# Optimization experiments

Measured on AMD Instinct MI355X. Metric: run time of the kernel, lower is better.

Reference implementation:

```python
import jax, jax.numpy as jnp
import numpy as np

B, S, E, H = 4, 2048, 512, 8
DH = E // H
EPS = 1e-5

def _ln(x, g, b):
    m = jnp.mean(x, axis=-1, keepdims=True)
    v = jnp.var(x, axis=-1, keepdims=True)
    return (x - m) * jax.lax.rsqrt(v + EPS) * g + b

def setup_inputs() -> dict:
    key = jax.random.key(0)
    ks = jax.random.split(key, 8)
    sc = 0.02
    return {
        "x": jax.random.normal(ks[0], (B, S, E), dtype=jnp.float32),
        "ln1_g": jnp.ones((E,), jnp.float32),
        "ln1_b": jnp.zeros((E,), jnp.float32),
        "in_proj_w": sc * jax.random.normal(ks[1], (3 * E, E), jnp.float32),
        "in_proj_b": jnp.zeros((3 * E,), jnp.float32),
        "out_w": sc * jax.random.normal(ks[2], (E, E), jnp.float32),
        "out_b": jnp.zeros((E,), jnp.float32),
        "ln2_g": jnp.ones((E,), jnp.float32),
        "ln2_b": jnp.zeros((E,), jnp.float32),
        "fc1_w": sc * jax.random.normal(ks[3], (E, E), jnp.float32),
        "fc1_b": jnp.zeros((E,), jnp.float32),
        "fc2_w": sc * jax.random.normal(ks[4], (E, E), jnp.float32),
        "fc2_b": jnp.zeros((E,), jnp.float32),
    }

def reference(x, ln1_g, ln1_b, in_proj_w, in_proj_b, out_w, out_b,
              ln2_g, ln2_b, fc1_w, fc1_b, fc2_w, fc2_b):
    # pre-LN
    z = _ln(x, ln1_g, ln1_b)
    # qkv projection (torch MHA packed in_proj: [3E, E])
    qkv = z @ in_proj_w.T + in_proj_b          # [B,S,3E]
    q, k, v = jnp.split(qkv, 3, axis=-1)
    q = q.reshape(B, S, H, DH)
    k = k.reshape(B, S, H, DH)
    v = v.reshape(B, S, H, DH)
    scores = jnp.einsum("bqhd,bkhd->bhqk", q, k) / np.sqrt(DH).astype(np.float32)
    causal = jnp.triu(jnp.ones((S, S), dtype=bool), k=1)  # True = masked
    neg = jnp.finfo(scores.dtype).min
    scores = jnp.where(causal, neg, scores)
    attn = jax.nn.softmax(scores, axis=-1)      # [B,H,S,S]
    ctx = jnp.einsum("bhqk,bkhd->bqhd", attn, v).reshape(B, S, E)
    attn_out = ctx @ out_w.T + out_b
    # torch MHA with need_weights=True averages over heads by default
    attn_weights = jnp.mean(attn, axis=1)       # [B,S,S]
    z2 = x + attn_out
    y = _ln(z2, ln2_g, ln2_b)
    y = jax.nn.leaky_relu(y @ fc1_w.T + fc1_b, negative_slope=0.01)
    y = y @ fc2_w.T + fc2_b
    y = y + z2
    return (y, attn_weights)
```

## Files before the change

kernel.cpp:

```cpp
#include <hip/hip_runtime.h>

typedef short bf16x8 __attribute__((ext_vector_type(8)));
typedef float f32x4 __attribute__((ext_vector_type(4)));
typedef unsigned short u16x8 __attribute__((ext_vector_type(8)));

#define NB 4
#define SQ 2048
#define EM 512
#define NH 8
#define DHD 64
#define QSCALE 0.1803368801111731f

__device__ __forceinline__ unsigned short f2bf(float x) {
  unsigned u = __float_as_uint(x);
  u += 0x7FFFu + ((u >> 16) & 1u);
  return (unsigned short)(u >> 16);
}

__device__ __forceinline__ int sw8(int row, int col8) { return col8 ^ ((row & 7) << 3); }

__global__ __launch_bounds__(256) void f2bf_kernel(const float* __restrict__ in,
                                                   unsigned short* __restrict__ out, int n) {
  int i = (blockIdx.x * 256 + threadIdx.x) * 8;
  if (i >= n) return;
  f32x4 a = *(const f32x4*)(in + i);
  f32x4 b = *(const f32x4*)(in + i + 4);
  u16x8 o;
#pragma unroll
  for (int j = 0; j < 4; ++j) { o[j] = f2bf(a[j]); o[j + 4] = f2bf(b[j]); }
  *(u16x8*)(out + i) = o;
}

__global__ __launch_bounds__(256) void ln_kernel(const float* __restrict__ x,
                                                 const float* __restrict__ g,
                                                 const float* __restrict__ bb,
                                                 unsigned short* __restrict__ out) {
  int tid = threadIdx.x;
  int row = blockIdx.x * 4 + (tid >> 6);
  int lane = tid & 63;
  size_t base = (size_t)row * EM + lane * 8;
  f32x4 v0 = *(const f32x4*)(x + base);
  f32x4 v1 = *(const f32x4*)(x + base + 4);
  float s = 0.f, q = 0.f;
#pragma unroll
  for (int j = 0; j < 4; ++j) { s += v0[j] + v1[j]; q += v0[j] * v0[j] + v1[j] * v1[j]; }
#pragma unroll
  for (int m = 1; m < 64; m <<= 1) { s += __shfl_xor(s, m); q += __shfl_xor(q, m); }
  float mean = s * (1.f / EM);
  float var = q * (1.f / EM) - mean * mean;
  float rs = rsqrtf(var + 1e-5f);
  f32x4 g0 = *(const f32x4*)(g + lane * 8), g1 = *(const f32x4*)(g + lane * 8 + 4);
  f32x4 b0 = *(const f32x4*)(bb + lane * 8), b1 = *(const f32x4*)(bb + lane * 8 + 4);
  u16x8 o;
#pragma unroll
  for (int j = 0; j < 4; ++j) {
    o[j] = f2bf((v0[j] - mean) * rs * g0[j] + b0[j]);
    o[j + 4] = f2bf((v1[j] - mean) * rs * g1[j] + b1[j]);
  }
  *(u16x8*)(out + base) = o;
}

template <bool LEAKY, bool RESID, bool OUTF32, bool QKV>
__global__ __launch_bounds__(256) void gemm64(
    const unsigned short* __restrict__ A, const unsigned short* __restrict__ Bm,
    const float* __restrict__ bias, const float* __restrict__ resid,
    float* __restrict__ outf, unsigned short* __restrict__ outh,
    unsigned short* __restrict__ qo, unsigned short* __restrict__ ko,
    unsigned short* __restrict__ vo, int M, int N, int K) {
  __shared__ unsigned short As[64][64];
  __shared__ unsigned short Bs[64][64];
  int m0 = blockIdx.x * 64, n0 = blockIdx.y * 64;
  int t = threadIdx.x;
  int ar = t >> 2, ac = (t & 3) * 16;
  int wv = t >> 6, ln = t & 63, lg = ln >> 4, lr = ln & 15;
  f32x4 acc[4];
#pragma unroll
  for (int c = 0; c < 4; ++c)
#pragma unroll
    for (int r = 0; r < 4; ++r) acc[c][r] = 0.f;

  const unsigned short* ag = A + (size_t)(m0 + ar) * K + ac;
  const unsigned short* bg = Bm + (size_t)(n0 + ar) * K + ac;
  for (int k0 = 0; k0 < K; k0 += 64) {
    u16x8 a0 = *(const u16x8*)(ag + k0);
    u16x8 a1 = *(const u16x8*)(ag + k0 + 8);
    u16x8 b0 = *(const u16x8*)(bg + k0);
    u16x8 b1 = *(const u16x8*)(bg + k0 + 8);
    *(u16x8*)&As[ar][sw8(ar, ac)] = a0;
    *(u16x8*)&As[ar][sw8(ar, ac + 8)] = a1;
    *(u16x8*)&Bs[ar][sw8(ar, ac)] = b0;
    *(u16x8*)&Bs[ar][sw8(ar, ac + 8)] = b1;
    __syncthreads();
#pragma unroll
    for (int kk = 0; kk < 64; kk += 32) {
      int arw = wv * 16 + lr;
      bf16x8 af = *(const bf16x8*)&As[arw][sw8(arw, kk + lg * 8)];
#pragma unroll
      for (int c = 0; c < 4; ++c) {
        int brw = c * 16 + lr;
        bf16x8 bf = *(const bf16x8*)&Bs[brw][sw8(brw, kk + lg * 8)];
        acc[c] = __builtin_amdgcn_mfma_f32_16x16x32_bf16(af, bf, acc[c], 0, 0, 0);
      }
    }
    __syncthreads();
  }
#pragma unroll
  for (int c = 0; c < 4; ++c) {
    int C_ = n0 + c * 16 + lr;
    float bv = bias[C_];
#pragma unroll
    for (int r = 0; r < 4; ++r) {
      int R_ = m0 + wv * 16 + lg * 4 + r;
      float v = acc[c][r] + bv;
      if (LEAKY) v = v > 0.f ? v : 0.01f * v;
      if (RESID) v += resid[(size_t)R_ * N + C_];
      if (QKV) {
        int which = C_ >> 9, f = C_ & 511, h = f >> 6, d = f & 63;
        int b_ = R_ >> 11, s_ = R_ & 2047;
        if (which == 0) {
          qo[(((size_t)b_ * NH + h) * SQ + s_) * DHD + d] = f2bf(v * QSCALE);
        } else if (which == 1) {
          ko[(((size_t)b_ * NH + h) * SQ + s_) * DHD + d] = f2bf(v);
        } else {
          vo[(((size_t)b_ * NH + h) * DHD + d) * SQ + s_] = f2bf(v);
        }
      } else if (OUTF32) {
        outf[(size_t)R_ * N + C_] = v;
      } else {
        outh[(size_t)R_ * N + C_] = f2bf(v);
      }
    }
  }
}

__global__ __launch_bounds__(256) void flash_kernel(
    const unsigned short* __restrict__ Q, const unsigned short* __restrict__ Kb,
    const unsigned short* __restrict__ Vt, unsigned short* __restrict__ ctx,
    float* __restrict__ mstat, float* __restrict__ lstat) {
  __shared__ unsigned short Ks[2][64][64];
  __shared__ unsigned short Vs[2][64][64];
  __shared__ unsigned short Ps[4][16][64];
  int h = blockIdx.y, b = blockIdx.z;
  int t = threadIdx.x, wv = t >> 6, ln = t & 63, lg = ln >> 4, lr = ln & 15;
  int ar = t >> 2, ac = (t & 3) * 16;
  size_t headoff = ((size_t)b * NH + h) * SQ;
  const unsigned short* kgb = Kb + (headoff + ar) * DHD + ac;
  const unsigned short* vgb = Vt + (((size_t)b * NH + h) * DHD + ar) * SQ + ac;

  bf16x8 vones;
#pragma unroll
  for (int j = 0; j < 8; ++j) vones[j] = (lr == 0) ? (short)0x3F80 : (short)0;

  for (int half = 0; half < 2; ++half) {
    int qt = half ? blockIdx.x : (31 - blockIdx.x);
    int qb = qt * 64;
    const unsigned short* qrow = Q + (headoff + qb + wv * 16 + lr) * DHD;
    bf16x8 aq0 = *(const bf16x8*)(qrow + lg * 8);
    bf16x8 aq1 = *(const bf16x8*)(qrow + 32 + lg * 8);

    f32x4 cacc[4], lacc;
#pragma unroll
    for (int nd = 0; nd < 4; ++nd)
#pragma unroll
      for (int r = 0; r < 4; ++r) cacc[nd][r] = 0.f;
#pragma unroll
    for (int r = 0; r < 4; ++r) lacc[r] = 0.f;
    float mrun[4];
#pragma unroll
    for (int r = 0; r < 4; ++r) mrun[r] = -__builtin_inff();

    int nkt = qt + 1;
    __syncthreads();
    u16x8 kr0 = *(const u16x8*)(kgb);
    u16x8 kr1 = *(const u16x8*)(kgb + 8);
    u16x8 vr0 = *(const u16x8*)(vgb);
    u16x8 vr1 = *(const u16x8*)(vgb + 8);
    *(u16x8*)&Ks[0][ar][sw8(ar, ac)] = kr0;
    *(u16x8*)&Ks[0][ar][sw8(ar, ac + 8)] = kr1;
    *(u16x8*)&Vs[0][ar][sw8(ar, ac)] = vr0;
    *(u16x8*)&Vs[0][ar][sw8(ar, ac + 8)] = vr1;
    if (nkt > 1) {
      kr0 = *(const u16x8*)(kgb + (size_t)64 * DHD);
      kr1 = *(const u16x8*)(kgb + (size_t)64 * DHD + 8);
      vr0 = *(const u16x8*)(vgb + 64);
      vr1 = *(const u16x8*)(vgb + 64 + 8);
    }

    for (int kt = 0; kt < nkt; ++kt) {
      int cur = kt & 1;
      __syncthreads();
      if (kt + 1 < nkt) {
        int nb = cur ^ 1;
        *(u16x8*)&Ks[nb][ar][sw8(ar, ac)] = kr0;
        *(u16x8*)&Ks[nb][ar][sw8(ar, ac + 8)] = kr1;
        *(u16x8*)&Vs[nb][ar][sw8(ar, ac)] = vr0;
        *(u16x8*)&Vs[nb][ar][sw8(ar, ac + 8)] = vr1;
        if (kt + 2 < nkt) {
          size_t ko2 = (size_t)(kt + 2) * 64;
          kr0 = *(const u16x8*)(kgb + ko2 * DHD);
          kr1 = *(const u16x8*)(kgb + ko2 * DHD + 8);
          vr0 = *(const u16x8*)(vgb + ko2);
          vr1 = *(const u16x8*)(vgb + ko2 + 8);
        }
      }

      float sv[4][4];
      __builtin_amdgcn_s_setprio(1);
#pragma unroll
      for (int nt = 0; nt < 4; ++nt) {
        f32x4 sf;
#pragma unroll
        for (int r = 0; r < 4; ++r) sf[r] = 0.f;
        int brw = nt * 16 + lr;
        bf16x8 bk0 = *(const bf16x8*)&Ks[cur][brw][sw8(brw, lg * 8)];
        bf16x8 bk1 = *(const bf16x8*)&Ks[cur][brw][sw8(brw, 32 + lg * 8)];
        sf = __builtin_amdgcn_mfma_f32_16x16x32_bf16(aq0, bk0, sf, 0, 0, 0);
        sf = __builtin_amdgcn_mfma_f32_16x16x32_bf16(aq1, bk1, sf, 0, 0, 0);
#pragma unroll
        for (int r = 0; r < 4; ++r) sv[nt][r] = sf[r];
      }
      __builtin_amdgcn_s_setprio(0);
      if (kt == nkt - 1) {
        int kbase = kt * 64;
#pragma unroll
        for (int nt = 0; nt < 4; ++nt) {
          int kcol = kbase + nt * 16 + lr;
#pragma unroll
          for (int r = 0; r < 4; ++r) {
            int qr = qb + wv * 16 + lg * 4 + r;
            if (kcol > qr) sv[nt][r] = -__builtin_inff();
          }
        }
      }

      float tmax[4], needmax = 0.f;
#pragma unroll
      for (int r = 0; r < 4; ++r) {
        float tm = fmaxf(fmaxf(sv[0][r], sv[1][r]), fmaxf(sv[2][r], sv[3][r]));
#pragma unroll
        for (int m = 1; m < 16; m <<= 1) tm = fmaxf(tm, __shfl_xor(tm, m));
        tmax[r] = tm;
        needmax = fmaxf(needmax, tm - mrun[r]);
      }
      if (__any(needmax > 8.f)) {
#pragma unroll
        for (int r = 0; r < 4; ++r) {
          float mn = fmaxf(mrun[r], tmax[r]);
          float sc = exp2f(mrun[r] - mn);
          mrun[r] = mn;
          lacc[r] *= sc;
#pragma unroll
          for (int nd = 0; nd < 4; ++nd) cacc[nd][r] *= sc;
        }
      }
#pragma unroll
      for (int r = 0; r < 4; ++r) {
        int prow = lg * 4 + r;
#pragma unroll
        for (int nt = 0; nt < 4; ++nt) {
          float p = exp2f(sv[nt][r] - mrun[r]);
          Ps[wv][prow][sw8(prow, nt * 16 + lr)] = f2bf(p);
        }
      }

      bf16x8 pf0 = *(const bf16x8*)&Ps[wv][lr][sw8(lr, lg * 8)];
      bf16x8 pf1 = *(const bf16x8*)&Ps[wv][lr][sw8(lr, 32 + lg * 8)];
      __builtin_amdgcn_s_setprio(1);
      lacc = __builtin_amdgcn_mfma_f32_16x16x32_bf16(pf0, vones, lacc, 0, 0, 0);
      lacc = __builtin_amdgcn_mfma_f32_16x16x32_bf16(pf1, vones, lacc, 0, 0, 0);
#pragma unroll
      for (int nd = 0; nd < 4; ++nd) {
        int vrw = nd * 16 + lr;
        bf16x8 vf0 = *(const bf16x8*)&Vs[cur][vrw][sw8(vrw, lg * 8)];
        bf16x8 vf1 = *(const bf16x8*)&Vs[cur][vrw][sw8(vrw, 32 + lg * 8)];
        cacc[nd] = __builtin_amdgcn_mfma_f32_16x16x32_bf16(pf0, vf0, cacc[nd], 0, 0, 0);
        cacc[nd] = __builtin_amdgcn_mfma_f32_16x16x32_bf16(pf1, vf1, cacc[nd], 0, 0, 0);
      }
      __builtin_amdgcn_s_setprio(0);
    }

    float inv[4];
#pragma unroll
    for (int r = 0; r < 4; ++r) inv[r] = 1.f / __shfl(lacc[r], ln & 48);
#pragma unroll
    for (int nd = 0; nd < 4; ++nd)
#pragma unroll
      for (int r = 0; r < 4; ++r) {
        size_t dst = ((size_t)b * SQ + qb + wv * 16 + lg * 4 + r) * EM + h * DHD + nd * 16 + lr;
        ctx[dst] = f2bf(cacc[nd][r] * inv[r]);
      }
    if (lr == 0) {
#pragma unroll
      for (int r = 0; r < 4; ++r) {
        int row = qb + wv * 16 + lg * 4 + r;
        mstat[headoff + row] = mrun[r];
        lstat[headoff + row] = 0.125f * inv[r];
      }
    }
  }
}

__global__ __launch_bounds__(256) void attnw_kernel(
    const unsigned short* __restrict__ Q, const unsigned short* __restrict__ Kb,
    const float* __restrict__ mstat, const float* __restrict__ lstat,
    float* __restrict__ aw) {
  int kt = blockIdx.x, qt = blockIdx.y, b = blockIdx.z;
  int qb = qt * 64, kb = kt * 64;
  int t = threadIdx.x;
  float* tile = aw + ((size_t)b * SQ + qb) * SQ + kb;
  if (kt > qt) {
    int row = t >> 2, c = (t & 3) * 16;
    f32x4 z;
#pragma unroll
    for (int j = 0; j < 4; ++j) z[j] = 0.f;
    float* p = tile + (size_t)row * SQ + c;
    *(f32x4*)p = z; *(f32x4*)(p + 4) = z; *(f32x4*)(p + 8) = z; *(f32x4*)(p + 12) = z;
    return;
  }
  __shared__ unsigned short Ks[2][64][64];
  int wv = t >> 6, ln = t & 63, lg = ln >> 4, lr = ln & 15;
  int sr = t >> 2, sc8 = (t & 3) * 16;
  bool diag = (kt == qt);
  size_t khstride = (size_t)SQ * DHD;
  const unsigned short* kg = Kb + (((size_t)b * NH) * SQ + kb + sr) * DHD + sc8;
  const unsigned short* qg = Q + (((size_t)b * NH) * SQ + qb + wv * 16 + lr) * DHD + lg * 8;
  size_t mbase = (size_t)b * NH * SQ + qb + wv * 16 + lg * 4;

  u16x8 ka = *(const u16x8*)kg;
  u16x8 kx = *(const u16x8*)(kg + 8);
  *(u16x8*)&Ks[0][sr][sw8(sr, sc8)] = ka;
  *(u16x8*)&Ks[0][sr][sw8(sr, sc8 + 8)] = kx;
  ka = *(const u16x8*)(kg + khstride);
  kx = *(const u16x8*)(kg + khstride + 8);

  bf16x8 aqc0 = *(const bf16x8*)qg;
  bf16x8 aqc1 = *(const bf16x8*)(qg + 32);
  bf16x8 aqn0 = *(const bf16x8*)(qg + khstride);
  bf16x8 aqn1 = *(const bf16x8*)(qg + khstride + 32);
  float mmc[4], lic[4], mmn[4], lin[4];
#pragma unroll
  for (int r = 0; r < 4; ++r) {
    mmc[r] = mstat[mbase + r];
    lic[r] = lstat[mbase + r];
    mmn[r] = mstat[mbase + SQ + r];
    lin[r] = lstat[mbase + SQ + r];
  }

  f32x4 facc[4];
#pragma unroll
  for (int nt = 0; nt < 4; ++nt)
#pragma unroll
    for (int r = 0; r < 4; ++r) facc[nt][r] = 0.f;

  for (int h = 0; h < NH; ++h) {
    int cur = h & 1;
    __syncthreads();
    if (h + 1 < NH) {
      *(u16x8*)&Ks[cur ^ 1][sr][sw8(sr, sc8)] = ka;
      *(u16x8*)&Ks[cur ^ 1][sr][sw8(sr, sc8 + 8)] = kx;
      if (h + 2 < NH) {
        ka = *(const u16x8*)(kg + (size_t)(h + 2) * khstride);
        kx = *(const u16x8*)(kg + (size_t)(h + 2) * khstride + 8);
      }
    }

#pragma unroll
    for (int nt = 0; nt < 4; ++nt) {
      f32x4 sf;
#pragma unroll
      for (int r = 0; r < 4; ++r) sf[r] = 0.f;
      int brw = nt * 16 + lr;
      bf16x8 bk0 = *(const bf16x8*)&Ks[cur][brw][sw8(brw, lg * 8)];
      bf16x8 bk1 = *(const bf16x8*)&Ks[cur][brw][sw8(brw, 32 + lg * 8)];
      sf = __builtin_amdgcn_mfma_f32_16x16x32_bf16(aqc0, bk0, sf, 0, 0, 0);
      sf = __builtin_amdgcn_mfma_f32_16x16x32_bf16(aqc1, bk1, sf, 0, 0, 0);
#pragma unroll
      for (int r = 0; r < 4; ++r) facc[nt][r] += exp2f(sf[r] - mmc[r]) * lic[r];
    }

    aqc0 = aqn0; aqc1 = aqn1;
#pragma unroll
    for (int r = 0; r < 4; ++r) { mmc[r] = mmn[r]; lic[r] = lin[r]; }
    if (h + 2 < NH) {
      aqn0 = *(const bf16x8*)(qg + (size_t)(h + 2) * khstride);
      aqn1 = *(const bf16x8*)(qg + (size_t)(h + 2) * khstride + 32);
#pragma unroll
      for (int r = 0; r < 4; ++r) {
        mmn[r] = mstat[mbase + (size_t)(h + 2) * SQ + r];
        lin[r] = lstat[mbase + (size_t)(h + 2) * SQ + r];
      }
    }
  }

#pragma unroll
  for (int nt = 0; nt < 4; ++nt) {
    int kc = kb + nt * 16 + lr;
#pragma unroll
    for (int r = 0; r < 4; ++r) {
      int qr = qb + wv * 16 + lg * 4 + r;
      float v = (diag && kc > qr) ? 0.f : facc[nt][r];
      tile[(size_t)(wv * 16 + lg * 4 + r) * SQ + nt * 16 + lr] = v;
    }
  }
}

extern "C" void kernel_launch(void* const* d_in, const int* in_sizes, int n_in,
                              void* d_out, int out_size, void* d_ws, size_t ws_size,
                              hipStream_t stream) {
  (void)in_sizes; (void)n_in; (void)out_size; (void)ws_size;
  const float* x = (const float*)d_in[0];
  const float* ln1g = (const float*)d_in[1];
  const float* ln1b = (const float*)d_in[2];
  const float* wqkv = (const float*)d_in[3];
  const float* bqkv = (const float*)d_in[4];
  const float* wout = (const float*)d_in[5];
  const float* bout = (const float*)d_in[6];
  const float* ln2g = (const float*)d_in[7];
  const float* ln2b = (const float*)d_in[8];
  const float* wfc1 = (const float*)d_in[9];
  const float* bfc1 = (const float*)d_in[10];
  const float* wfc2 = (const float*)d_in[11];
  const float* bfc2 = (const float*)d_in[12];

  char* ws = (char*)d_ws;
  unsigned short* zctx = (unsigned short*)(ws);
  unsigned short* qb_ = (unsigned short*)(ws + 8388608);
  unsigned short* kb_ = (unsigned short*)(ws + 16777216);
  unsigned short* vb_ = (unsigned short*)(ws + 25165824);
  float* z2 = (float*)(ws + 33554432);
  float* mstat = (float*)(ws + 50331648);
  float* lstat = (float*)(ws + 50593792);
  unsigned short* wqkv_h = (unsigned short*)(ws + 50855936);
  unsigned short* wout_h = (unsigned short*)(ws + 52428800);
  unsigned short* wfc1_h = (unsigned short*)(ws + 52953088);
  unsigned short* wfc2_h = (unsigned short*)(ws + 53477376);
  unsigned short* y1 = qb_;
  unsigned short* h1 = kb_;

  float* outy = (float*)d_out;
  float* outw = outy + (size_t)NB * SQ * EM;

  f2bf_kernel<<<384, 256, 0, stream>>>(wqkv, wqkv_h, 786432);
  f2bf_kernel<<<128, 256, 0, stream>>>(wout, wout_h, 262144);
  f2bf_kernel<<<128, 256, 0, stream>>>(wfc1, wfc1_h, 262144);
  f2bf_kernel<<<128, 256, 0, stream>>>(wfc2, wfc2_h, 262144);

  ln_kernel<<<2048, 256, 0, stream>>>(x, ln1g, ln1b, zctx);
  gemm64<false, false, false, true><<<dim3(128, 24), 256, 0, stream>>>(
      zctx, wqkv_h, bqkv, nullptr, nullptr, nullptr, qb_, kb_, vb_, 8192, 1536, 512);
  flash_kernel<<<dim3(16, 8, 4), 256, 0, stream>>>(qb_, kb_, vb_, zctx, mstat, lstat);
  attnw_kernel<<<dim3(32, 32, 4), 256, 0, stream>>>(qb_, kb_, mstat, lstat, outw);
  gemm64<false, true, true, false><<<dim3(128, 8), 256, 0, stream>>>(
      zctx, wout_h, bout, x, z2, nullptr, nullptr, nullptr, nullptr, 8192, 512, 512);
  ln_kernel<<<2048, 256, 0, stream>>>(z2, ln2g, ln2b, y1);
  gemm64<true, false, false, false><<<dim3(128, 8), 256, 0, stream>>>(
      y1, wfc1_h, bfc1, nullptr, nullptr, h1, nullptr, nullptr, nullptr, 8192, 512, 512);
  gemm64<false, true, true, false><<<dim3(128, 8), 256, 0, stream>>>(
      h1, wfc2_h, bfc2, z2, outy, nullptr, nullptr, nullptr, nullptr, 8192, 512, 512);
}
```

Baseline: 204.0 us.

## Split flash attention KV range across two wave groups and merge partials

The flash kernel now gives each block a single query tile with 512 threads. Two groups of four waves each process half of the causal KV tiles, and their partial softmax statistics and outputs are merged through LDS at the end. This replaces the old scheme of one 256-thread block handling two paired query tiles in sequence, which doubles the grid and aims to raise parallelism and shorten the critical path. The rescale check now compares per-lane maxima before doing the cross-lane shuffle, so the shuffle is skipped when no rescale is needed. The costs are 80KB of LDS per block, an extra merge pass with two barriers, and an idle group on the smallest tiles.

New measurement: 218.0 us. 1.07x slower.

```diff
diff --git a/kernel.cpp b/kernel.cpp
--- a/kernel.cpp
+++ b/kernel.cpp
@@ -133,167 +133,218 @@
   }
 }
 
-__global__ __launch_bounds__(256) void flash_kernel(
+__global__ __launch_bounds__(512, 4) void flash_kernel(
     const unsigned short* __restrict__ Q, const unsigned short* __restrict__ Kb,
     const unsigned short* __restrict__ Vt, unsigned short* __restrict__ ctx,
     float* __restrict__ mstat, float* __restrict__ lstat) {
-  __shared__ unsigned short Ks[2][64][64];
-  __shared__ unsigned short Vs[2][64][64];
-  __shared__ unsigned short Ps[4][16][64];
+  __shared__ __attribute__((aligned(16))) char lds[81920];
+  int qt = 31 - blockIdx.x;
   int h = blockIdx.y, b = blockIdx.z;
-  int t = threadIdx.x, wv = t >> 6, ln = t & 63, lg = ln >> 4, lr = ln & 15;
-  int ar = t >> 2, ac = (t & 3) * 16;
+  int qb = qt * 64;
+  int t = threadIdx.x;
+  int wv = t >> 6, ln = t & 63, lg = ln >> 4, lr = ln & 15;
+  int g = wv >> 2, wg = wv & 3;
+  int ts = t & 255, ar = ts >> 2, ac = (ts & 3) * 16;
   size_t headoff = ((size_t)b * NH + h) * SQ;
   const unsigned short* kgb = Kb + (headoff + ar) * DHD + ac;
   const unsigned short* vgb = Vt + (((size_t)b * NH + h) * DHD + ar) * SQ + ac;
+  unsigned short(*Ps)[64] = (unsigned short(*)[64])(lds + 65536 + wv * 2048);
+
+  const unsigned short* qrow = Q + (headoff + qb + wg * 16 + lr) * DHD;
+  bf16x8 aq0 = *(const bf16x8*)(qrow + lg * 8);
+  bf16x8 aq1 = *(const bf16x8*)(qrow + 32 + lg * 8);
 
   bf16x8 vones;
 #pragma unroll
   for (int j = 0; j < 8; ++j) vones[j] = (lr == 0) ? (short)0x3F80 : (short)0;
 
-  for (int half = 0; half < 2; ++half) {
-    int qt = half ? blockIdx.x : (31 - blockIdx.x);
-    int qb = qt * 64;
-    const unsigned short* qrow = Q + (headoff + qb + wv * 16 + lr) * DHD;
-    bf16x8 aq0 = *(const bf16x8*)(qrow + lg * 8);
-    bf16x8 aq1 = *(const bf16x8*)(qrow + 32 + lg * 8);
-
-    f32x4 cacc[4], lacc;
+  f32x4 cacc[4], lacc;
+#pragma unroll
+  for (int nd = 0; nd < 4; ++nd)
+#pragma unroll
+    for (int r = 0; r < 4; ++r) cacc[nd][r] = 0.f;
+#pragma unroll
+  for (int r = 0; r < 4; ++r) lacc[r] = 0.f;
+  float mrun[4];
+#pragma unroll
+  for (int r = 0; r < 4; ++r) mrun[r] = -__builtin_inff();
+
+  int nkt = qt + 1;
+  int split = (nkt + 1) >> 1;
+  int k0 = g ? split : 0;
+  int myCnt = g ? (nkt - split) : split;
+
+  u16x8 kr0, kr1, vr0, vr1;
+  if (myCnt > 0) {
+    const unsigned short* kp = kgb + (size_t)(k0 * 64) * DHD;
+    kr0 = *(const u16x8*)kp;
+    kr1 = *(const u16x8*)(kp + 8);
+    vr0 = *(const u16x8*)(vgb + k0 * 64);
+    vr1 = *(const u16x8*)(vgb + k0 * 64 + 8);
+    unsigned short(*K0)[64] = (unsigned short(*)[64])(lds + g * 32768);
+    unsigned short(*V0)[64] = (unsigned short(*)[64])(lds + g * 32768 + 16384);
+    *(u16x8*)&K0[ar][sw8(ar, ac)] = kr0;
+    *(u16x8*)&K0[ar][sw8(ar, ac + 8)] = kr1;
+    *(u16x8*)&V0[ar][sw8(ar, ac)] = vr0;
+    *(u16x8*)&V0[ar][sw8(ar, ac + 8)] = vr1;
+    if (myCnt > 1) {
+      const unsigned short* kp1 = kgb + (size_t)((k0 + 1) * 64) * DHD;
+      kr0 = *(const u16x8*)kp1;
+      kr1 = *(const u16x8*)(kp1 + 8);
+      vr0 = *(const u16x8*)(vgb + (k0 + 1) * 64);
+      vr1 = *(const u16x8*)(vgb + (k0 + 1) * 64 + 8);
+    }
+  }
+
+  for (int i = 0; i < split; ++i) {
+    int cur = i & 1;
+    __syncthreads();
+    bool act = i < myCnt;
+    if (act && i + 1 < myCnt) {
+      char* nb = lds + g * 32768 + (cur ^ 1) * 8192;
+      unsigned short(*Kn)[64] = (unsigned short(*)[64])nb;
+      unsigned short(*Vn)[64] = (unsigned short(*)[64])(nb + 16384);
+      *(u16x8*)&Kn[ar][sw8(ar, ac)] = kr0;
+      *(u16x8*)&Kn[ar][sw8(ar, ac + 8)] = kr1;
+      *(u16x8*)&Vn[ar][sw8(ar, ac)] = vr0;
+      *(u16x8*)&Vn[ar][sw8(ar, ac + 8)] = vr1;
+      if (i + 2 < myCnt) {
+        size_t ko2 = (size_t)((k0 + i + 2) * 64);
+        kr0 = *(const u16x8*)(kgb + ko2 * DHD);
+        kr1 = *(const u16x8*)(kgb + ko2 * DHD + 8);
+        vr0 = *(const u16x8*)(vgb + ko2);
+        vr1 = *(const u16x8*)(vgb + ko2 + 8);
+      }
+    }
+    if (!act) continue;
+    int kt = k0 + i;
+    char* cb = lds + g * 32768 + cur * 8192;
+    unsigned short(*Kc)[64] = (unsigned short(*)[64])cb;
+    unsigned short(*Vc)[64] = (unsigned short(*)[64])(cb + 16384);
+
+    float sv[4][4];
+    __builtin_amdgcn_s_setprio(1);
+#pragma unroll
+    for (int nt = 0; nt < 4; ++nt) {
+      f32x4 sf;
+#pragma unroll
+      for (int r = 0; r < 4; ++r) sf[r] = 0.f;
+      int brw = nt * 16 + lr;
+      bf16x8 bk0 = *(const bf16x8*)&Kc[brw][sw8(brw, lg * 8)];
+      bf16x8 bk1 = *(const bf16x8*)&Kc[brw][sw8(brw, 32 + lg * 8)];
+      sf = __builtin_amdgcn_mfma_f32_16x16x32_bf16(aq0, bk0, sf, 0, 0, 0);
+      sf = __builtin_amdgcn_mfma_f32_16x16x32_bf16(aq1, bk1, sf, 0, 0, 0);
+#pragma unroll
+      for (int r = 0; r < 4; ++r) sv[nt][r] = sf[r];
+    }
+    __builtin_amdgcn_s_setprio(0);
+    if (kt == nkt - 1) {
+      int kbase = kt * 64;
+#pragma unroll
+      for (int nt = 0; nt < 4; ++nt) {
+        int kcol = kbase + nt * 16 + lr;
+#pragma unroll
+        for (int r = 0; r < 4; ++r) {
+          int qr = qb + wg * 16 + lg * 4 + r;
+          if (kcol > qr) sv[nt][r] = -__builtin_inff();
+        }
+      }
+    }
+
+    float lmax[4];
+    bool need = false;
+#pragma unroll
+    for (int r = 0; r < 4; ++r) {
+      lmax[r] = fmaxf(fmaxf(sv[0][r], sv[1][r]), fmaxf(sv[2][r], sv[3][r]));
+      need |= (lmax[r] > mrun[r] + 8.f);
+    }
+    if (__any(need)) {
+#pragma unroll
+      for (int r = 0; r < 4; ++r) {
+        float tm = lmax[r];
+#pragma unroll
+        for (int m = 1; m < 16; m <<= 1) tm = fmaxf(tm, __shfl_xor(tm, m));
+        float mn = fmaxf(mrun[r], tm);
+        float sc = exp2f(mrun[r] - mn);
+        mrun[r] = mn;
+        lacc[r] *= sc;
+#pragma unroll
+        for (int nd = 0; nd < 4; ++nd) cacc[nd][r] *= sc;
+      }
+    }
+#pragma unroll
+    for (int r = 0; r < 4; ++r) {
+      int prow = lg * 4 + r;
+#pragma unroll
+      for (int nt = 0; nt < 4; ++nt) {
+        float p = exp2f(sv[nt][r] - mrun[r]);
+        Ps[prow][sw8(prow, nt * 16 + lr)] = f2bf(p);
+      }
+    }
+
+    bf16x8 pf0 = *(const bf16x8*)&Ps[lr][sw8(lr, lg * 8)];
+    bf16x8 pf1 = *(const bf16x8*)&Ps[lr][sw8(lr, 32 + lg * 8)];
+    __builtin_amdgcn_s_setprio(1);
+    lacc = __builtin_amdgcn_mfma_f32_16x16x32_bf16(pf0, vones, lacc, 0, 0, 0);
+    lacc = __builtin_amdgcn_mfma_f32_16x16x32_bf16(pf1, vones, lacc, 0, 0, 0);
+#pragma unroll
+    for (int nd = 0; nd < 4; ++nd) {
+      int vrw = nd * 16 + lr;
+      bf16x8 vf0 = *(const bf16x8*)&Vc[vrw][sw8(vrw, lg * 8)];
+      bf16x8 vf1 = *(const bf16x8*)&Vc[vrw][sw8(vrw, 32 + lg * 8)];
+      cacc[nd] = __builtin_amdgcn_mfma_f32_16x16x32_bf16(pf0, vf0, cacc[nd], 0, 0, 0);
+      cacc[nd] = __builtin_amdgcn_mfma_f32_16x16x32_bf16(pf1, vf1, cacc[nd], 0, 0, 0);
+    }
+    __builtin_amdgcn_s_setprio(0);
+  }
+
+  float* red = (float*)lds;
+  float* m1buf = (float*)(lds + 17408);
+  float* l1buf = (float*)(lds + 17664);
+  __syncthreads();
+  if (g == 1) {
 #pragma unroll
     for (int nd = 0; nd < 4; ++nd)
 #pragma unroll
-      for (int r = 0; r < 4; ++r) cacc[nd][r] = 0.f;
-#pragma unroll
-    for (int r = 0; r < 4; ++r) lacc[r] = 0.f;
-    float mrun[4];
-#pragma unroll
-    for (int r = 0; r < 4; ++r) mrun[r] = -__builtin_inff();
-
-    int nkt = qt + 1;
-    __syncthreads();
-    u16x8 kr0 = *(const u16x8*)(kgb);
-    u16x8 kr1 = *(const u16x8*)(kgb + 8);
-    u16x8 vr0 = *(const u16x8*)(vgb);
-    u16x8 vr1 = *(const u16x8*)(vgb + 8);
-    *(u16x8*)&Ks[0][ar][sw8(ar, ac)] = kr0;
-    *(u16x8*)&Ks[0][ar][sw8(ar, ac + 8)] = kr1;
-    *(u16x8*)&Vs[0][ar][sw8(ar, ac)] = vr0;
-    *(u16x8*)&Vs[0][ar][sw8(ar, ac + 8)] = vr1;
-    if (nkt > 1) {
-      kr0 = *(const u16x8*)(kgb + (size_t)64 * DHD);
-      kr1 = *(const u16x8*)(kgb + (size_t)64 * DHD + 8);
-      vr0 = *(const u16x8*)(vgb + 64);
-      vr1 = *(const u16x8*)(vgb + 64 + 8);
-    }
-
-    for (int kt = 0; kt < nkt; ++kt) {
-      int cur = kt & 1;
-      __syncthreads();
-      if (kt + 1 < nkt) {
-        int nb = cur ^ 1;
-        *(u16x8*)&Ks[nb][ar][sw8(ar, ac)] = kr0;
-        *(u16x8*)&Ks[nb][ar][sw8(ar, ac + 8)] = kr1;
-        *(u16x8*)&Vs[nb][ar][sw8(ar, ac)] = vr0;
-        *(u16x8*)&Vs[nb][ar][sw8(ar, ac + 8)] = vr1;
-        if (kt + 2 < nkt) {
-          size_t ko2 = (size_t)(kt + 2) * 64;
-          kr0 = *(const u16x8*)(kgb + ko2 * DHD);
-          kr1 = *(const u16x8*)(kgb + ko2 * DHD + 8);
-          vr0 = *(const u16x8*)(vgb + ko2);
-          vr1 = *(const u16x8*)(vgb + ko2 + 8);
-        }
-      }
-
-      float sv[4][4];
-      __builtin_amdgcn_s_setprio(1);
-#pragma unroll
-      for (int nt = 0; nt < 4; ++nt) {
-        f32x4 sf;
-#pragma unroll
-        for (int r = 0; r < 4; ++r) sf[r] = 0.f;
-        int brw = nt * 16 + lr;
-        bf16x8 bk0 = *(const bf16x8*)&Ks[cur][brw][sw8(brw, lg * 8)];
-        bf16x8 bk1 = *(const bf16x8*)&Ks[cur][brw][sw8(brw, 32 + lg * 8)];
-        sf = __builtin_amdgcn_mfma_f32_16x16x32_bf16(aq0, bk0, sf, 0, 0, 0);
-        sf = __builtin_amdgcn_mfma_f32_16x16x32_bf16(aq1, bk1, sf, 0, 0, 0);
-#pragma unroll
-        for (int r = 0; r < 4; ++r) sv[nt][r] = sf[r];
-      }
-      __builtin_amdgcn_s_setprio(0);
-      if (kt == nkt - 1) {
-        int kbase = kt * 64;
-#pragma unroll
-        for (int nt = 0; nt < 4; ++nt) {
-          int kcol = kbase + nt * 16 + lr;
-#pragma unroll
-          for (int r = 0; r < 4; ++r) {
-            int qr = qb + wv * 16 + lg * 4 + r;
-            if (kcol > qr) sv[nt][r] = -__builtin_inff();
-          }
-        }
-      }
-
-      float tmax[4], needmax = 0.f;
+      for (int r = 0; r < 4; ++r)
+        red[(wg * 16 + lg * 4 + r) * 68 + nd * 16 + lr] = cacc[nd][r];
+    if (lr == 0) {
 #pragma unroll
       for (int r = 0; r < 4; ++r) {
-        float tm = fmaxf(fmaxf(sv[0][r], sv[1][r]), fmaxf(sv[2][r], sv[3][r]));
-#pragma unroll
-        for (int m = 1; m < 16; m <<= 1) tm = fmaxf(tm, __shfl_xor(tm, m));
-        tmax[r] = tm;
-        needmax = fmaxf(needmax, tm - mrun[r]);
-      }
-      if (__any(needmax > 8.f)) {
-#pragma unroll
-        for (int r = 0; r < 4; ++r) {
-          float mn = fmaxf(mrun[r], tmax[r]);
-          float sc = exp2f(mrun[r] - mn);
-          mrun[r] = mn;
-          lacc[r] *= sc;
-#pragma unroll
-          for (int nd = 0; nd < 4; ++nd) cacc[nd][r] *= sc;
-        }
-      }
+        m1buf[wg * 16 + lg * 4 + r] = mrun[r];
+        l1buf[wg * 16 + lg * 4 + r] = lacc[r];
+      }
+    }
+  }
+  __syncthreads();
+  if (g == 0) {
+    float inv[4], sc0[4], sc1[4], mfin[4];
+#pragma unroll
+    for (int r = 0; r < 4; ++r) {
+      int row = wg * 16 + lg * 4 + r;
+      float l0 = __shfl(lacc[r], ln & 48);
+      float m1 = m1buf[row], l1 = l1buf[row];
+      float mm = fmaxf(mrun[r], m1);
+      sc0[r] = exp2f(mrun[r] - mm);
+      sc1[r] = exp2f(m1 - mm);
+      float lf = l0 * sc0[r] + l1 * sc1[r];
+      inv[r] = 1.f / lf;
+      mfin[r] = mm;
+    }
+#pragma unroll
+    for (int nd = 0; nd < 4; ++nd)
 #pragma unroll
       for (int r = 0; r < 4; ++r) {
-        int prow = lg * 4 + r;
-#pragma unroll
-        for (int nt = 0; nt < 4; ++nt) {
-          float p = exp2f(sv[nt][r] - mrun[r]);
-          Ps[wv][prow][sw8(prow, nt * 16 + lr)] = f2bf(p);
-        }
-      }
-
-      bf16x8 pf0 = *(const bf16x8*)&Ps[wv][lr][sw8(lr, lg * 8)];
-      bf16x8 pf1 = *(const bf16x8*)&Ps[wv][lr][sw8(lr, 32 + lg * 8)];
-      __builtin_amdgcn_s_setprio(1);
-      lacc = __builtin_amdgcn_mfma_f32_16x16x32_bf16(pf0, vones, lacc, 0, 0, 0);
-      lacc = __builtin_amdgcn_mfma_f32_16x16x32_bf16(pf1, vones, lacc, 0, 0, 0);
-#pragma unroll
-      for (int nd = 0; nd < 4; ++nd) {
-        int vrw = nd * 16 + lr;
-        bf16x8 vf0 = *(const bf16x8*)&Vs[cur][vrw][sw8(vrw, lg * 8)];
-        bf16x8 vf1 = *(const bf16x8*)&Vs[cur][vrw][sw8(vrw, 32 + lg * 8)];
-        cacc[nd] = __builtin_amdgcn_mfma_f32_16x16x32_bf16(pf0, vf0, cacc[nd], 0, 0, 0);
-        cacc[nd] = __builtin_amdgcn_mfma_f32_16x16x32_bf16(pf1, vf1, cacc[nd], 0, 0, 0);
-      }
-      __builtin_amdgcn_s_setprio(0);
-    }
-
-    float inv[4];
-#pragma unroll
-    for (int r = 0; r < 4; ++r) inv[r] = 1.f / __shfl(lacc[r], ln & 48);
-#pragma unroll
-    for (int nd = 0; nd < 4; ++nd)
+        int row = wg * 16 + lg * 4 + r;
+        float o = cacc[nd][r] * sc0[r] + red[row * 68 + nd * 16 + lr] * sc1[r];
+        size_t dst = ((size_t)b * SQ + qb + row) * EM + h * DHD + nd * 16 + lr;
+        ctx[dst] = f2bf(o * inv[r]);
+      }
+    if (lr == 0) {
 #pragma unroll
       for (int r = 0; r < 4; ++r) {
-        size_t dst = ((size_t)b * SQ + qb + wv * 16 + lg * 4 + r) * EM + h * DHD + nd * 16 + lr;
-        ctx[dst] = f2bf(cacc[nd][r] * inv[r]);
-      }
-    if (lr == 0) {
-#pragma unroll
-      for (int r = 0; r < 4; ++r) {
-        int row = qb + wv * 16 + lg * 4 + r;
-        mstat[headoff + row] = mrun[r];
+        int row = qb + wg * 16 + lg * 4 + r;
+        mstat[headoff + row] = mfin[r];
         lstat[headoff + row] = 0.125f * inv[r];
       }
     }
@@ -448,7 +499,7 @@
   ln_kernel<<<2048, 256, 0, stream>>>(x, ln1g, ln1b, zctx);
   gemm64<false, false, false, true><<<dim3(128, 24), 256, 0, stream>>>(
       zctx, wqkv_h, bqkv, nullptr, nullptr, nullptr, qb_, kb_, vb_, 8192, 1536, 512);
-  flash_kernel<<<dim3(16, 8, 4), 256, 0, stream>>>(qb_, kb_, vb_, zctx, mstat, lstat);
+  flash_kernel<<<dim3(32, 8, 4), 512, 0, stream>>>(qb_, kb_, vb_, zctx, mstat, lstat);
   attnw_kernel<<<dim3(32, 32, 4), 256, 0, stream>>>(qb_, kb_, mstat, lstat, outw);
   gemm64<false, true, true, false><<<dim3(128, 8), 256, 0, stream>>>(
       zctx, wout_h, bout, x, z2, nullptr, nullptr, nullptr, nullptr, 8192, 512, 512);
```

## Split flash attention into paired 32-row query tiles sharing K/V loads

Applied to the files above, without the earlier changes.

Each flash block used to process two 64-row query tiles one after the other. Now each block covers two 32-row query tiles at once, a short and a long one, with two waves on each. The K/V tiles are loaded into shared memory once for both, and the waves on the shorter tile skip compute once they are done. The grid doubles to raise parallelism and balance causal work. Separately, the cross-lane max shuffles now run only when a lane's partial max exceeds the running max threshold, which cuts shuffle work per key tile. The risk is that waves on the short tile sit idle while the long tile finishes.

Measured after the change: 232.4 us. +14.0%, slower.

```diff
diff --git a/kernel.cpp b/kernel.cpp
--- a/kernel.cpp
+++ b/kernel.cpp
@@ -140,162 +140,164 @@
   __shared__ unsigned short Ks[2][64][64];
   __shared__ unsigned short Vs[2][64][64];
   __shared__ unsigned short Ps[4][16][64];
+  int i = blockIdx.x;
   int h = blockIdx.y, b = blockIdx.z;
+  int hi = 63 - i;
   int t = threadIdx.x, wv = t >> 6, ln = t & 63, lg = ln >> 4, lr = ln & 15;
   int ar = t >> 2, ac = (t & 3) * 16;
+  int qt32 = (wv < 2) ? hi : i;
+  int myCnt = (qt32 >> 1) + 1;
+  int maxCnt = (hi >> 1) + 1;
+  int qrow0 = qt32 * 32 + (wv & 1) * 16;
   size_t headoff = ((size_t)b * NH + h) * SQ;
   const unsigned short* kgb = Kb + (headoff + ar) * DHD + ac;
   const unsigned short* vgb = Vt + (((size_t)b * NH + h) * DHD + ar) * SQ + ac;
 
+  const unsigned short* qrow = Q + (headoff + qrow0 + lr) * DHD;
+  bf16x8 aq0 = *(const bf16x8*)(qrow + lg * 8);
+  bf16x8 aq1 = *(const bf16x8*)(qrow + 32 + lg * 8);
+
   bf16x8 vones;
 #pragma unroll
   for (int j = 0; j < 8; ++j) vones[j] = (lr == 0) ? (short)0x3F80 : (short)0;
 
-  for (int half = 0; half < 2; ++half) {
-    int qt = half ? blockIdx.x : (31 - blockIdx.x);
-    int qb = qt * 64;
-    const unsigned short* qrow = Q + (headoff + qb + wv * 16 + lr) * DHD;
-    bf16x8 aq0 = *(const bf16x8*)(qrow + lg * 8);
-    bf16x8 aq1 = *(const bf16x8*)(qrow + 32 + lg * 8);
-
-    f32x4 cacc[4], lacc;
-#pragma unroll
-    for (int nd = 0; nd < 4; ++nd)
-#pragma unroll
-      for (int r = 0; r < 4; ++r) cacc[nd][r] = 0.f;
-#pragma unroll
-    for (int r = 0; r < 4; ++r) lacc[r] = 0.f;
-    float mrun[4];
-#pragma unroll
-    for (int r = 0; r < 4; ++r) mrun[r] = -__builtin_inff();
-
-    int nkt = qt + 1;
+  f32x4 cacc[4], lacc;
+#pragma unroll
+  for (int nd = 0; nd < 4; ++nd)
+#pragma unroll
+    for (int r = 0; r < 4; ++r) cacc[nd][r] = 0.f;
+#pragma unroll
+  for (int r = 0; r < 4; ++r) lacc[r] = 0.f;
+  float mrun[4];
+#pragma unroll
+  for (int r = 0; r < 4; ++r) mrun[r] = -__builtin_inff();
+
+  u16x8 kr0 = *(const u16x8*)(kgb);
+  u16x8 kr1 = *(const u16x8*)(kgb + 8);
+  u16x8 vr0 = *(const u16x8*)(vgb);
+  u16x8 vr1 = *(const u16x8*)(vgb + 8);
+  *(u16x8*)&Ks[0][ar][sw8(ar, ac)] = kr0;
+  *(u16x8*)&Ks[0][ar][sw8(ar, ac + 8)] = kr1;
+  *(u16x8*)&Vs[0][ar][sw8(ar, ac)] = vr0;
+  *(u16x8*)&Vs[0][ar][sw8(ar, ac + 8)] = vr1;
+  if (maxCnt > 1) {
+    kr0 = *(const u16x8*)(kgb + (size_t)64 * DHD);
+    kr1 = *(const u16x8*)(kgb + (size_t)64 * DHD + 8);
+    vr0 = *(const u16x8*)(vgb + 64);
+    vr1 = *(const u16x8*)(vgb + 64 + 8);
+  }
+
+  for (int kt = 0; kt < maxCnt; ++kt) {
+    int cur = kt & 1;
     __syncthreads();
-    u16x8 kr0 = *(const u16x8*)(kgb);
-    u16x8 kr1 = *(const u16x8*)(kgb + 8);
-    u16x8 vr0 = *(const u16x8*)(vgb);
-    u16x8 vr1 = *(const u16x8*)(vgb + 8);
-    *(u16x8*)&Ks[0][ar][sw8(ar, ac)] = kr0;
-    *(u16x8*)&Ks[0][ar][sw8(ar, ac + 8)] = kr1;
-    *(u16x8*)&Vs[0][ar][sw8(ar, ac)] = vr0;
-    *(u16x8*)&Vs[0][ar][sw8(ar, ac + 8)] = vr1;
-    if (nkt > 1) {
-      kr0 = *(const u16x8*)(kgb + (size_t)64 * DHD);
-      kr1 = *(const u16x8*)(kgb + (size_t)64 * DHD + 8);
-      vr0 = *(const u16x8*)(vgb + 64);
-      vr1 = *(const u16x8*)(vgb + 64 + 8);
-    }
-
-    for (int kt = 0; kt < nkt; ++kt) {
-      int cur = kt & 1;
-      __syncthreads();
-      if (kt + 1 < nkt) {
-        int nb = cur ^ 1;
-        *(u16x8*)&Ks[nb][ar][sw8(ar, ac)] = kr0;
-        *(u16x8*)&Ks[nb][ar][sw8(ar, ac + 8)] = kr1;
-        *(u16x8*)&Vs[nb][ar][sw8(ar, ac)] = vr0;
-        *(u16x8*)&Vs[nb][ar][sw8(ar, ac + 8)] = vr1;
-        if (kt + 2 < nkt) {
-          size_t ko2 = (size_t)(kt + 2) * 64;
-          kr0 = *(const u16x8*)(kgb + ko2 * DHD);
-          kr1 = *(const u16x8*)(kgb + ko2 * DHD + 8);
-          vr0 = *(const u16x8*)(vgb + ko2);
-          vr1 = *(const u16x8*)(vgb + ko2 + 8);
+    if (kt + 1 < maxCnt) {
+      int nb = cur ^ 1;
+      *(u16x8*)&Ks[nb][ar][sw8(ar, ac)] = kr0;
+      *(u16x8*)&Ks[nb][ar][sw8(ar, ac + 8)] = kr1;
+      *(u16x8*)&Vs[nb][ar][sw8(ar, ac)] = vr0;
+      *(u16x8*)&Vs[nb][ar][sw8(ar, ac + 8)] = vr1;
+      if (kt + 2 < maxCnt) {
+        size_t ko2 = (size_t)(kt + 2) * 64;
+        kr0 = *(const u16x8*)(kgb + ko2 * DHD);
+        kr1 = *(const u16x8*)(kgb + ko2 * DHD + 8);
+        vr0 = *(const u16x8*)(vgb + ko2);
+        vr1 = *(const u16x8*)(vgb + ko2 + 8);
+      }
+    }
+    if (kt >= myCnt) continue;
+
+    float sv[4][4];
+    __builtin_amdgcn_s_setprio(1);
+#pragma unroll
+    for (int nt = 0; nt < 4; ++nt) {
+      f32x4 sf;
+#pragma unroll
+      for (int r = 0; r < 4; ++r) sf[r] = 0.f;
+      int brw = nt * 16 + lr;
+      bf16x8 bk0 = *(const bf16x8*)&Ks[cur][brw][sw8(brw, lg * 8)];
+      bf16x8 bk1 = *(const bf16x8*)&Ks[cur][brw][sw8(brw, 32 + lg * 8)];
+      sf = __builtin_amdgcn_mfma_f32_16x16x32_bf16(aq0, bk0, sf, 0, 0, 0);
+      sf = __builtin_amdgcn_mfma_f32_16x16x32_bf16(aq1, bk1, sf, 0, 0, 0);
+#pragma unroll
+      for (int r = 0; r < 4; ++r) sv[nt][r] = sf[r];
+    }
+    __builtin_amdgcn_s_setprio(0);
+    if (kt == myCnt - 1) {
+      int kbase = kt * 64;
+#pragma unroll
+      for (int nt = 0; nt < 4; ++nt) {
+        int kcol = kbase + nt * 16 + lr;
+#pragma unroll
+        for (int r = 0; r < 4; ++r) {
+          int qr = qrow0 + lg * 4 + r;
+          if (kcol > qr) sv[nt][r] = -__builtin_inff();
         }
       }
-
-      float sv[4][4];
-      __builtin_amdgcn_s_setprio(1);
+    }
+
+    float lmax[4];
+    bool need = false;
+#pragma unroll
+    for (int r = 0; r < 4; ++r) {
+      lmax[r] = fmaxf(fmaxf(sv[0][r], sv[1][r]), fmaxf(sv[2][r], sv[3][r]));
+      need |= (lmax[r] > mrun[r] + 8.f);
+    }
+    if (__any(need)) {
+#pragma unroll
+      for (int r = 0; r < 4; ++r) {
+        float tm = lmax[r];
+#pragma unroll
+        for (int m = 1; m < 16; m <<= 1) tm = fmaxf(tm, __shfl_xor(tm, m));
+        float mn = fmaxf(mrun[r], tm);
+        float sc = exp2f(mrun[r] - mn);
+        mrun[r] = mn;
+        lacc[r] *= sc;
+#pragma unroll
+        for (int nd = 0; nd < 4; ++nd) cacc[nd][r] *= sc;
+      }
+    }
+#pragma unroll
+    for (int r = 0; r < 4; ++r) {
+      int prow = lg * 4 + r;
 #pragma unroll
       for (int nt = 0; nt < 4; ++nt) {
-        f32x4 sf;
-#pragma unroll
-        for (int r = 0; r < 4; ++r) sf[r] = 0.f;
-        int brw = nt * 16 + lr;
-        bf16x8 bk0 = *(const bf16x8*)&Ks[cur][brw][sw8(brw, lg * 8)];
-        bf16x8 bk1 = *(const bf16x8*)&Ks[cur][brw][sw8(brw, 32 + lg * 8)];
-        sf = __builtin_amdgcn_mfma_f32_16x16x32_bf16(aq0, bk0, sf, 0, 0, 0);
-        sf = __builtin_amdgcn_mfma_f32_16x16x32_bf16(aq1, bk1, sf, 0, 0, 0);
-#pragma unroll
-        for (int r = 0; r < 4; ++r) sv[nt][r] = sf[r];
-      }
-      __builtin_amdgcn_s_setprio(0);
-      if (kt == nkt - 1) {
-        int kbase = kt * 64;
-#pragma unroll
-        for (int nt = 0; nt < 4; ++nt) {
-          int kcol = kbase + nt * 16 + lr;
-#pragma unroll
-          for (int r = 0; r < 4; ++r) {
-            int qr = qb + wv * 16 + lg * 4 + r;
-            if (kcol > qr) sv[nt][r] = -__builtin_inff();
-          }
-        }
-      }
-
-      float tmax[4], needmax = 0.f;
-#pragma unroll
-      for (int r = 0; r < 4; ++r) {
-        float tm = fmaxf(fmaxf(sv[0][r], sv[1][r]), fmaxf(sv[2][r], sv[3][r]));
-#pragma unroll
-        for (int m = 1; m < 16; m <<= 1) tm = fmaxf(tm, __shfl_xor(tm, m));
-        tmax[r] = tm;
-        needmax = fmaxf(needmax, tm - mrun[r]);
-      }
-      if (__any(needmax > 8.f)) {
-#pragma unroll
-        for (int r = 0; r < 4; ++r) {
-          float mn = fmaxf(mrun[r], tmax[r]);
-          float sc = exp2f(mrun[r] - mn);
-          mrun[r] = mn;
-          lacc[r] *= sc;
-#pragma unroll
-          for (int nd = 0; nd < 4; ++nd) cacc[nd][r] *= sc;
-        }
-      }
-#pragma unroll
-      for (int r = 0; r < 4; ++r) {
-        int prow = lg * 4 + r;
-#pragma unroll
-        for (int nt = 0; nt < 4; ++nt) {
-          float p = exp2f(sv[nt][r] - mrun[r]);
-          Ps[wv][prow][sw8(prow, nt * 16 + lr)] = f2bf(p);
-        }
-      }
-
-      bf16x8 pf0 = *(const bf16x8*)&Ps[wv][lr][sw8(lr, lg * 8)];
-      bf16x8 pf1 = *(const bf16x8*)&Ps[wv][lr][sw8(lr, 32 + lg * 8)];
-      __builtin_amdgcn_s_setprio(1);
-      lacc = __builtin_amdgcn_mfma_f32_16x16x32_bf16(pf0, vones, lacc, 0, 0, 0);
-      lacc = __builtin_amdgcn_mfma_f32_16x16x32_bf16(pf1, vones, lacc, 0, 0, 0);
-#pragma unroll
-      for (int nd = 0; nd < 4; ++nd) {
-        int vrw = nd * 16 + lr;
-        bf16x8 vf0 = *(const bf16x8*)&Vs[cur][vrw][sw8(vrw, lg * 8)];
-        bf16x8 vf1 = *(const bf16x8*)&Vs[cur][vrw][sw8(vrw, 32 + lg * 8)];
-        cacc[nd] = __builtin_amdgcn_mfma_f32_16x16x32_bf16(pf0, vf0, cacc[nd], 0, 0, 0);
-        cacc[nd] = __builtin_amdgcn_mfma_f32_16x16x32_bf16(pf1, vf1, cacc[nd], 0, 0, 0);
-      }
-      __builtin_amdgcn_s_setprio(0);
-    }
-
-    float inv[4];
-#pragma unroll
-    for (int r = 0; r < 4; ++r) inv[r] = 1.f / __shfl(lacc[r], ln & 48);
-#pragma unroll
-    for (int nd = 0; nd < 4; ++nd)
-#pragma unroll
-      for (int r = 0; r < 4; ++r) {
-        size_t dst = ((size_t)b * SQ + qb + wv * 16 + lg * 4 + r) * EM + h * DHD + nd * 16 + lr;
-        ctx[dst] = f2bf(cacc[nd][r] * inv[r]);
-      }
-    if (lr == 0) {
-#pragma unroll
-      for (int r = 0; r < 4; ++r) {
-        int row = qb + wv * 16 + lg * 4 + r;
-        mstat[headoff + row] = mrun[r];
-        lstat[headoff + row] = 0.125f * inv[r];
-      }
+        float p = exp2f(sv[nt][r] - mrun[r]);
+        Ps[wv][prow][sw8(prow, nt * 16 + lr)] = f2bf(p);
+      }
+    }
+
+    bf16x8 pf0 = *(const bf16x8*)&Ps[wv][lr][sw8(lr, lg * 8)];
+    bf16x8 pf1 = *(const bf16x8*)&Ps[wv][lr][sw8(lr, 32 + lg * 8)];
+    __builtin_amdgcn_s_setprio(1);
+    lacc = __builtin_amdgcn_mfma_f32_16x16x32_bf16(pf0, vones, lacc, 0, 0, 0);
+    lacc = __builtin_amdgcn_mfma_f32_16x16x32_bf16(pf1, vones, lacc, 0, 0, 0);
+#pragma unroll
+    for (int nd = 0; nd < 4; ++nd) {
+      int vrw = nd * 16 + lr;
+      bf16x8 vf0 = *(const bf16x8*)&Vs[cur][vrw][sw8(vrw, lg * 8)];
+      bf16x8 vf1 = *(const bf16x8*)&Vs[cur][vrw][sw8(vrw, 32 + lg * 8)];
+      cacc[nd] = __builtin_amdgcn_mfma_f32_16x16x32_bf16(pf0, vf0, cacc[nd], 0, 0, 0);
+      cacc[nd] = __builtin_amdgcn_mfma_f32_16x16x32_bf16(pf1, vf1, cacc[nd], 0, 0, 0);
+    }
+    __builtin_amdgcn_s_setprio(0);
+  }
+
+  float inv[4];
+#pragma unroll
+  for (int r = 0; r < 4; ++r) inv[r] = 1.f / __shfl(lacc[r], ln & 48);
+#pragma unroll
+  for (int nd = 0; nd < 4; ++nd)
+#pragma unroll
+    for (int r = 0; r < 4; ++r) {
+      size_t dst = ((size_t)b * SQ + qrow0 + lg * 4 + r) * EM + h * DHD + nd * 16 + lr;
+      ctx[dst] = f2bf(cacc[nd][r] * inv[r]);
+    }
+  if (lr == 0) {
+#pragma unroll
+    for (int r = 0; r < 4; ++r) {
+      int row = qrow0 + lg * 4 + r;
+      mstat[headoff + row] = mrun[r];
+      lstat[headoff + row] = 0.125f * inv[r];
     }
   }
 }
@@ -448,7 +450,7 @@
   ln_kernel<<<2048, 256, 0, stream>>>(x, ln1g, ln1b, zctx);
   gemm64<false, false, false, true><<<dim3(128, 24), 256, 0, stream>>>(
       zctx, wqkv_h, bqkv, nullptr, nullptr, nullptr, qb_, kb_, vb_, 8192, 1536, 512);
-  flash_kernel<<<dim3(16, 8, 4), 256, 0, stream>>>(qb_, kb_, vb_, zctx, mstat, lstat);
+  flash_kernel<<<dim3(32, 8, 4), 256, 0, stream>>>(qb_, kb_, vb_, zctx, mstat, lstat);
   attnw_kernel<<<dim3(32, 32, 4), 256, 0, stream>>>(qb_, kb_, mstat, lstat, outw);
   gemm64<false, true, true, false><<<dim3(128, 8), 256, 0, stream>>>(
       zctx, wout_h, bout, x, z2, nullptr, nullptr, nullptr, nullptr, 8192, 512, 512);
```
